# Performance work log

Hardware: AMD Instinct MI355X
Metric: run time of the kernel (lower is better)

## Reference

```python
import jax, jax.numpy as jnp
import numpy as np

B, U, HEADS, S = 16, 1024, 8, 1024


def setup_inputs() -> dict:
    key = jax.random.key(0)
    k1, k2, k3, k4 = jax.random.split(key, 4)
    x = jax.random.normal(k1, (B, U, S), dtype=jnp.float32)
    mask = jax.random.randint(k2, (B, S, S), 0, 2).astype(bool)
    w_qkv = jax.random.normal(k3, (3 * U, U), dtype=jnp.float32) * 0.02
    w_out = jax.random.normal(k4, (U, U), dtype=jnp.float32) * 0.02
    return {"x": x, "mask": mask, "w_qkv": w_qkv, "w_out": w_out}


def reference(x, mask, w_qkv, w_out):
    # x: (B, U, S), mask: (B, n_queries, n_keys) bool
    b, u, s = x.shape
    h = HEADS
    c = u // h  # head (chunk) size
    scale = 1.0 / np.sqrt(c).astype(np.float32)

    # 1x1-conv QKV projection (bias=False): (3U, U) x (B, U, S) -> (B, 3U, S)
    qkv = jnp.einsum('ou,bus->bos', w_qkv, x)
    Q, K, V = jnp.split(qkv, 3, axis=1)           # each (B, U, S)
    Qh = Q.reshape(b, h, c, s)
    Kh = K.reshape(b, h, c, s)
    Vh = V.reshape(b, h, c, s)

    # attention logits: (B, H, n_q, n_k)
    A = jnp.einsum('bhcq,bhck->bhqk', Qh, Kh)

    # relu activation with per-query valid-key-count normalization
    m = mask.sum(axis=2)[:, :, None]              # (B, n_q, 1) count of valid keys
    n_elem = jnp.where(mask, m, 1).astype(A.dtype)[:, None]  # (B, 1, n_q, n_k)
    mask_b = mask[:, None]                        # broadcast over heads
    A = jnp.where(mask_b, jax.nn.relu(A) * scale, -jnp.inf)
    A = A / n_elem
    A = jnp.where(jnp.isinf(A), jnp.zeros((), A.dtype), A)

    # attention-value aggregation (faithful math of broadcast+sum): (B, H, C, n_q)
    Ch = jnp.einsum('bhqk,bhck->bhcq', A, Vh)
    Cc = Ch.reshape(b, u, s)

    # finishing 1x1-conv linear layer
    return jnp.einsum('ou,bus->bos', w_out, Cc)
```

## Files before the change

### kernel.cpp

```cpp
#include <hip/hip_runtime.h>

#define B_DIM 16
#define U_DIM 1024
#define H_DIM 8
#define S_DIM 1024
#define C_DIM 128
#define KD 1024
#define SCALE 0.08838834764831845f

typedef __attribute__((ext_vector_type(8))) short s16x8;
typedef __attribute__((ext_vector_type(4))) float f32x4;

__device__ __forceinline__ void gll16(const void* g, void* l) {
  __builtin_amdgcn_global_load_lds(
      (const __attribute__((address_space(1))) unsigned int*)g,
      (__attribute__((address_space(3))) unsigned int*)l, 16, 0, 0);
}
__device__ __forceinline__ unsigned short f2bf(float f) {
  unsigned u = __float_as_uint(f);
  u += 0x7FFF + ((u >> 16) & 1u);
  return (unsigned short)(u >> 16);
}
#define MFMA16(a, b, c) __builtin_amdgcn_mfma_f32_16x16x32_bf16(a, b, c, 0, 0, 0)

__global__ void detect_mask(const unsigned char* __restrict__ mask_raw, int* __restrict__ flag) {
  __shared__ int not01, notf;
  if (threadIdx.x == 0) { not01 = 0; notf = 0; }
  __syncthreads();
  const unsigned int* p = (const unsigned int*)mask_raw;
  int l01 = 0, lf = 0;
  for (int i = threadIdx.x; i < 4096; i += 256) {
    unsigned int v = p[i];
    if (v != 0u && v != 1u) l01 = 1;
    if (v != 0u && v != 0x3F800000u) lf = 1;
  }
  if (l01) atomicOr(&not01, 1);
  if (lf) atomicOr(&notf, 1);
  __syncthreads();
  if (threadIdx.x == 0) flag[0] = (!not01) ? 0 : ((!notf) ? 2 : 1);
}

__global__ __launch_bounds__(256) void pack_mask(const unsigned char* __restrict__ mask_raw,
                                                 const int* __restrict__ flag,
                                                 unsigned long long* __restrict__ bits) {
  __shared__ unsigned char tile[64][80];
  const int t = threadIdx.x;
  const int kt = blockIdx.x * 64, qw = blockIdx.y, b = blockIdx.z;
  const int mk = flag[0];
  const int q = t >> 2, kbase = (t & 3) * 16;
  const size_t row = (size_t)(b * S_DIM + qw * 64 + q);
  if (mk == 1) {
    uint4 v = *(const uint4*)(mask_raw + (row << 10) + kt + kbase);
    *(uint4*)&tile[q][kbase] = v;
  } else if (mk == 0) {
    const int* p = (const int*)mask_raw + (row << 10) + kt + kbase;
#pragma unroll
    for (int j = 0; j < 4; ++j) {
      int4 v = ((const int4*)p)[j];
      uchar4 o;
      o.x = v.x ? 1 : 0; o.y = v.y ? 1 : 0; o.z = v.z ? 1 : 0; o.w = v.w ? 1 : 0;
      *(uchar4*)&tile[q][kbase + j * 4] = o;
    }
  } else {
    const float* p = (const float*)mask_raw + (row << 10) + kt + kbase;
#pragma unroll
    for (int j = 0; j < 4; ++j) {
      float4 v = ((const float4*)p)[j];
      uchar4 o;
      o.x = (v.x != 0.f) ? 1 : 0; o.y = (v.y != 0.f) ? 1 : 0;
      o.z = (v.z != 0.f) ? 1 : 0; o.w = (v.w != 0.f) ? 1 : 0;
      *(uchar4*)&tile[q][kbase + j * 4] = o;
    }
  }
  __syncthreads();
  const int wave = t >> 6, lane = t & 63;
#pragma unroll
  for (int qq = 0; qq < 16; ++qq) {
    int qr = wave * 16 + qq;
    unsigned long long bal = __ballot(tile[qr][lane] != 0);
    if (lane == 0)
      bits[(size_t)blockIdx.x * (B_DIM * S_DIM) + (size_t)b * S_DIM + qw * 64 + qr] = bal;
  }
}

__global__ __launch_bounds__(256) void invm_from_bits(const unsigned long long* __restrict__ bits,
                                                      float* __restrict__ invm) {
  int idx = blockIdx.x * 256 + threadIdx.x;
  int s = 0;
#pragma unroll
  for (int kt = 0; kt < S_DIM / 64; ++kt)
    s += __popcll(bits[(size_t)kt * (B_DIM * S_DIM) + idx]);
  invm[idx] = (s > 0) ? (SCALE / (float)s) : 0.f;
}

__global__ __launch_bounds__(256) void cvt_bf16(const float* __restrict__ in,
                                                unsigned short* __restrict__ out, int n) {
  int i = (blockIdx.x * 256 + threadIdx.x) * 4;
  if (i < n) {
    float4 v = *(const float4*)(in + i);
    ushort4 o;
    o.x = f2bf(v.x); o.y = f2bf(v.y); o.z = f2bf(v.z); o.w = f2bf(v.w);
    *(ushort4*)(out + i) = o;
  }
}

__global__ __launch_bounds__(256) void transpose_x(const float* __restrict__ x,
                                                   unsigned short* __restrict__ xT) {
  __shared__ float T[32][33];
  const int t = threadIdx.x, r = t >> 3, c4 = (t & 7) * 4;
  const int s0 = blockIdx.x * 32, u0 = blockIdx.y * 32;
  const size_t base = (size_t)blockIdx.z * U_DIM * S_DIM;
  float4 v = *(const float4*)(x + base + (size_t)(u0 + r) * S_DIM + s0 + c4);
  T[r][c4 + 0] = v.x; T[r][c4 + 1] = v.y; T[r][c4 + 2] = v.z; T[r][c4 + 3] = v.w;
  __syncthreads();
  ushort4 o;
  o.x = f2bf(T[c4 + 0][r]); o.y = f2bf(T[c4 + 1][r]);
  o.z = f2bf(T[c4 + 2][r]); o.w = f2bf(T[c4 + 3][r]);
  *(ushort4*)(xT + base + (size_t)(s0 + r) * U_DIM + u0 + c4) = o;
}

__global__ __launch_bounds__(256) void transpose_v(const unsigned short* __restrict__ qkvT,
                                                   unsigned short* __restrict__ VT) {
  __shared__ unsigned short T[32][34];
  const int t = threadIdx.x, r = t >> 3, c4 = (t & 7) * 4;
  const int k0 = blockIdx.x * 32, c0 = blockIdx.y * 32;
  const unsigned short* qb = qkvT + (size_t)blockIdx.z * S_DIM * (3 * U_DIM);
  ushort4 v = *(const ushort4*)(qb + (size_t)(k0 + r) * (3 * U_DIM) + 2 * U_DIM + c0 + c4);
  T[r][c4 + 0] = v.x; T[r][c4 + 1] = v.y; T[r][c4 + 2] = v.z; T[r][c4 + 3] = v.w;
  __syncthreads();
  ushort4 o;
  o.x = T[c4 + 0][r]; o.y = T[c4 + 1][r]; o.z = T[c4 + 2][r]; o.w = T[c4 + 3][r];
  *(ushort4*)(VT + (size_t)blockIdx.z * U_DIM * S_DIM + (size_t)(c0 + r) * S_DIM + k0 + c4) = o;
}

template <typename OUT>
__global__ __launch_bounds__(256) void gemm_tt(const unsigned short* __restrict__ A,
                                               const unsigned short* __restrict__ Bm,
                                               OUT* __restrict__ D,
                                               long long sAb, long long sBb, long long sDb,
                                               int N) {
  __shared__ unsigned short sA[128 * 64];
  __shared__ unsigned short sB[128 * 64];
  const int tid = threadIdx.x, wave = tid >> 6, lane = tid & 63;
  const int l15 = lane & 15, quad = lane >> 4;
  const unsigned int Lb = blockIdx.x + gridDim.x * (blockIdx.y + gridDim.y * blockIdx.z);
  const unsigned int nwg = gridDim.x * gridDim.y * gridDim.z;
  const unsigned int logical = (Lb & 7u) * (nwg >> 3) + (Lb >> 3);
  const int bx = logical % gridDim.x;
  const unsigned int rem = logical / gridDim.x;
  const int by = rem % gridDim.y;
  const int bz = rem / gridDim.y;
  const int m0 = by * 128, n0 = bx * 128;
  A += (size_t)bz * sAb;
  Bm += (size_t)bz * sBb;
  D += (size_t)bz * sDb;
  const int wm = (wave >> 1) * 64, wn = (wave & 1) * 64;
  f32x4 acc[4][4] = {};

  for (int k0 = 0; k0 < KD; k0 += 64) {
#pragma unroll
    for (int t = 0; t < 4; ++t) {
      int p = wave * 256 + t * 64 + lane;
      int row = p >> 3, kc = (p & 7) ^ (row & 7);
      gll16(A + (size_t)(m0 + row) * KD + k0 + kc * 8, &sA[(wave * 256 + t * 64) * 8]);
    }
#pragma unroll
    for (int t = 0; t < 4; ++t) {
      int p = wave * 256 + t * 64 + lane;
      int row = p >> 3, kc = (p & 7) ^ (row & 7);
      gll16(Bm + (size_t)(n0 + row) * KD + k0 + kc * 8, &sB[(wave * 256 + t * 64) * 8]);
    }
    __syncthreads();
#pragma unroll
    for (int kk = 0; kk < 2; ++kk) {
      s16x8 af[4], bf[4];
#pragma unroll
      for (int i = 0; i < 4; ++i) {
        int row = wm + i * 16 + l15;
        af[i] = *(const s16x8*)&sA[row * 64 + ((kk * 4 + quad) ^ (row & 7)) * 8];
      }
#pragma unroll
      for (int j = 0; j < 4; ++j) {
        int row = wn + j * 16 + l15;
        bf[j] = *(const s16x8*)&sB[row * 64 + ((kk * 4 + quad) ^ (row & 7)) * 8];
      }
#pragma unroll
      for (int i = 0; i < 4; ++i)
#pragma unroll
        for (int j = 0; j < 4; ++j) acc[i][j] = MFMA16(af[i], bf[j], acc[i][j]);
    }
    __syncthreads();
  }
#pragma unroll
  for (int i = 0; i < 4; ++i)
#pragma unroll
    for (int j = 0; j < 4; ++j) {
      f32x4 v = acc[i][j];
#pragma unroll
      for (int r = 0; r < 4; ++r) {
        int m = m0 + wm + i * 16 + quad * 4 + r;
        int n = n0 + wn + j * 16 + l15;
        if constexpr (sizeof(OUT) == 2) D[(size_t)m * N + n] = f2bf(v[r]);
        else D[(size_t)m * N + n] = v[r];
      }
    }
}

__global__ __launch_bounds__(256, 2) void attn_mfma(const unsigned short* __restrict__ qkvT,
                                                    const unsigned short* __restrict__ VT,
                                                    const unsigned long long* __restrict__ bits,
                                                    const float* __restrict__ invm,
                                                    unsigned short* __restrict__ CcT, int b0) {
  __shared__ unsigned short QV[64 * 128];
  __shared__ unsigned short Ks[64 * 128];
  __shared__ unsigned short Vs[128 * 64];
  __shared__ unsigned short Ps[64 * 64];
  __shared__ float invs[64];

  const int tid = threadIdx.x, wave = tid >> 6, lane = tid & 63;
  const int l15 = lane & 15, quad = lane >> 4;
  const int L = blockIdx.x + 16 * (blockIdx.y + 8 * blockIdx.z);
  const int cpx = (16 * H_DIM * gridDim.z) >> 3;
  const int logical = (L & 7) * cpx + (L >> 3);
  const int qt = logical & 15, h = (logical >> 4) & 7, z = logical >> 7;
  const int q0 = qt * 64, b = b0 + z;
  const unsigned short* qB = qkvT + (size_t)z * S_DIM * (3 * U_DIM);
  const unsigned short* Vb = VT + (size_t)z * U_DIM * S_DIM + (size_t)h * C_DIM * S_DIM;

#pragma unroll
  for (int t = 0; t < 4; ++t) {
    int p = wave * 256 + t * 64 + lane;
    int row = p >> 4, c = (p & 15) ^ (row & 7);
    gll16(qB + (size_t)(q0 + row) * (3 * U_DIM) + h * C_DIM + c * 8,
          &QV[(wave * 256 + t * 64) * 8]);
    gll16(qB + (size_t)(row) * (3 * U_DIM) + U_DIM + h * C_DIM + c * 8,
          &Ks[(wave * 256 + t * 64) * 8]);
    int vrow = p >> 3, vkc = (p & 7) ^ (vrow & 7);
    gll16(Vb + (size_t)vrow * S_DIM + vkc * 8, &Vs[(wave * 256 + t * 64) * 8]);
  }
  if (tid < 64) invs[tid] = invm[(size_t)b * S_DIM + q0 + tid];
  __syncthreads();

  s16x8 qf[4][4];
#pragma unroll
  for (int j = 0; j < 4; ++j)
#pragma unroll
    for (int kk = 0; kk < 4; ++kk) {
      int row = j * 16 + l15;
      qf[j][kk] = *(const s16x8*)&QV[row * 128 + ((kk * 4 + quad) ^ (row & 7)) * 8];
    }
  float invf[4];
#pragma unroll
  for (int j = 0; j < 4; ++j) invf[j] = invs[j * 16 + l15];

  f32x4 pacc[4][2] = {};

  for (int kt = 0; kt < S_DIM / 64; ++kt) {
    unsigned long long w64[4];
    {
      const unsigned long long* mw =
          bits + (size_t)kt * (B_DIM * S_DIM) + (size_t)b * S_DIM + q0;
#pragma unroll
      for (int j = 0; j < 4; ++j) w64[j] = mw[j * 16 + l15];
    }

    s16x8 af[4];
#pragma unroll
    for (int kk = 0; kk < 4; ++kk) {
      int row = wave * 16 + l15;
      af[kk] = *(const s16x8*)&Ks[row * 128 + ((kk * 4 + quad) ^ (row & 7)) * 8];
    }
    f32x4 sacc[4] = {};
    __builtin_amdgcn_s_setprio(1);
#pragma unroll
    for (int kk = 0; kk < 4; ++kk)
#pragma unroll
      for (int j = 0; j < 4; ++j) sacc[j] = MFMA16(af[kk], qf[j][kk], sacc[j]);
    __builtin_amdgcn_s_setprio(0);

#pragma unroll
    for (int j = 0; j < 4; ++j) {
      const unsigned int m4 = (unsigned int)(w64[j] >> (wave * 16 + quad * 4)) & 0xFu;
      float p[4];
#pragma unroll
      for (int r = 0; r < 4; ++r) {
        float t = fmaxf(sacc[j][r], 0.f) * invf[j];
        p[r] = ((m4 >> r) & 1u) ? t : 0.f;
      }
      unsigned int pk0, pk1;
      asm("v_cvt_pk_bf16_f32 %0, %1, %2" : "=v"(pk0) : "v"(p[0]), "v"(p[1]));
      asm("v_cvt_pk_bf16_f32 %0, %1, %2" : "=v"(pk1) : "v"(p[2]), "v"(p[3]));
      int q = j * 16 + l15;
      int chunk = (wave * 2 + (quad >> 1)) ^ (q & 7);
      *(uint2*)&Ps[q * 64 + chunk * 8 + (quad & 1) * 4] = make_uint2(pk0, pk1);
    }
    __syncthreads();

    if (kt < S_DIM / 64 - 1) {
      const int kn = (kt + 1) * 64;
      unsigned short* vdst = (kt & 1) ? Vs : QV;
#pragma unroll
      for (int t = 0; t < 4; ++t) {
        int p = wave * 256 + t * 64 + lane;
        int row = p >> 4, c = (p & 15) ^ (row & 7);
        gll16(qB + (size_t)(kn + row) * (3 * U_DIM) + U_DIM + h * C_DIM + c * 8,
              &Ks[(wave * 256 + t * 64) * 8]);
        int vrow = p >> 3, vkc = (p & 7) ^ (vrow & 7);
        gll16(Vb + (size_t)vrow * S_DIM + kn + vkc * 8, &vdst[(wave * 256 + t * 64) * 8]);
      }
    }

    const unsigned short* vbuf = (kt & 1) ? QV : Vs;
#pragma unroll
    for (int ks = 0; ks < 2; ++ks) {
      s16x8 pf[4], vf[2];
#pragma unroll
      for (int i = 0; i < 4; ++i) {
        int row = i * 16 + l15;
        pf[i] = *(const s16x8*)&Ps[row * 64 + ((ks * 4 + quad) ^ (row & 7)) * 8];
      }
#pragma unroll
      for (int j = 0; j < 2; ++j) {
        int row = wave * 32 + j * 16 + l15;
        vf[j] = *(const s16x8*)&vbuf[row * 64 + ((ks * 4 + quad) ^ (row & 7)) * 8];
      }
      __builtin_amdgcn_s_setprio(1);
#pragma unroll
      for (int i = 0; i < 4; ++i)
#pragma unroll
        for (int j = 0; j < 2; ++j) pacc[i][j] = MFMA16(pf[i], vf[j], pacc[i][j]);
      __builtin_amdgcn_s_setprio(0);
    }
    __syncthreads();
  }

  unsigned short* cb = CcT + (size_t)z * S_DIM * U_DIM;
#pragma unroll
  for (int i = 0; i < 4; ++i)
#pragma unroll
    for (int j = 0; j < 2; ++j) {
      f32x4 v = pacc[i][j];
#pragma unroll
      for (int r = 0; r < 4; ++r) {
        int q = q0 + i * 16 + quad * 4 + r;
        int c = h * C_DIM + wave * 32 + j * 16 + l15;
        cb[(size_t)q * U_DIM + c] = f2bf(v[r]);
      }
    }
}

extern "C" void kernel_launch(void* const* d_in, const int* in_sizes, int n_in,
                              void* d_out, int out_size, void* d_ws, size_t ws_size,
                              hipStream_t stream) {
  const float* x = (const float*)d_in[0];
  const unsigned char* mask_raw = (const unsigned char*)d_in[1];
  const float* w_qkv = (const float*)d_in[2];
  const float* w_out = (const float*)d_in[3];
  float* out = (float*)d_out;

  char* ws = (char*)d_ws;
  int* flag = (int*)ws;
  float* invm = (float*)(ws + 256);
  unsigned long long* bits = (unsigned long long*)(ws + 256 + 65536);
  unsigned short* wqkv_bf = (unsigned short*)((char*)bits + (size_t)B_DIM * S_DIM * 16 * 8);
  unsigned short* wout_bf = (unsigned short*)((char*)wqkv_bf + (size_t)3 * U_DIM * U_DIM * 2);
  char* heap = (char*)wout_bf + (size_t)U_DIM * U_DIM * 2;

  const size_t xT_pb = (size_t)U_DIM * S_DIM * 2;
  const size_t qkvT_pb = (size_t)3 * U_DIM * S_DIM * 2;
  const size_t vT_pb = (size_t)U_DIM * S_DIM * 2;
  const size_t ccT_pb = (size_t)U_DIM * S_DIM * 2;
  const size_t per_batch = xT_pb + qkvT_pb + vT_pb + ccT_pb;
  const size_t fixed = (size_t)(heap - ws);
  int nb = (ws_size > fixed) ? (int)((ws_size - fixed) / per_batch) : 1;
  if (nb < 1) nb = 1;
  if (nb > B_DIM) nb = B_DIM;

  unsigned short* xT = (unsigned short*)heap;
  unsigned short* qkvT = (unsigned short*)(heap + (size_t)nb * xT_pb);
  unsigned short* VT = (unsigned short*)(heap + (size_t)nb * (xT_pb + qkvT_pb));
  unsigned short* CcT = (unsigned short*)(heap + (size_t)nb * (xT_pb + qkvT_pb + vT_pb));

  detect_mask<<<1, 256, 0, stream>>>(mask_raw, flag);
  pack_mask<<<dim3(S_DIM / 64, S_DIM / 64, B_DIM), 256, 0, stream>>>(mask_raw, flag, bits);
  invm_from_bits<<<(B_DIM * S_DIM) / 256, 256, 0, stream>>>(bits, invm);
  cvt_bf16<<<(3 * U_DIM * U_DIM) / 1024, 256, 0, stream>>>(w_qkv, wqkv_bf, 3 * U_DIM * U_DIM);
  cvt_bf16<<<(U_DIM * U_DIM) / 1024, 256, 0, stream>>>(w_out, wout_bf, U_DIM * U_DIM);

  for (int b0 = 0; b0 < B_DIM; b0 += nb) {
    int cnt = (B_DIM - b0 < nb) ? (B_DIM - b0) : nb;
    transpose_x<<<dim3(S_DIM / 32, U_DIM / 32, cnt), 256, 0, stream>>>(
        x + (size_t)b0 * U_DIM * S_DIM, xT);
    gemm_tt<unsigned short><<<dim3(3 * U_DIM / 128, S_DIM / 128, cnt), 256, 0, stream>>>(
        xT, wqkv_bf, qkvT, (long long)U_DIM * S_DIM, 0LL, (long long)3 * U_DIM * S_DIM, 3 * U_DIM);
    transpose_v<<<dim3(S_DIM / 32, U_DIM / 32, cnt), 256, 0, stream>>>(qkvT, VT);
    attn_mfma<<<dim3(S_DIM / 64, H_DIM, cnt), 256, 0, stream>>>(
        qkvT, VT, bits, invm, CcT, b0);
    gemm_tt<float><<<dim3(S_DIM / 128, U_DIM / 128, cnt), 256, 0, stream>>>(
        wout_bf, CcT, out + (size_t)b0 * U_DIM * S_DIM, 0LL,
        (long long)U_DIM * S_DIM, (long long)U_DIM * S_DIM, S_DIM);
  }
}
```

Before: 484.7 us.

## Replace GEMMs with 256x256-tile, 512-thread, triple-buffered LDS pipeline

Both projection GEMMs move from a 128x128-tile, 256-thread kernel that loads and syncs every K step to a 256x256-tile, 512-thread kernel. The new kernel uses K=32 stages held in three LDS buffers, prefetched two steps ahead with partial vmcnt waits. It also raises wave priority around the MFMA block. The goal is to hide global-to-LDS latency behind compute and get more operand reuse per tile, at the cost of 96KB LDS, more accumulator registers, and fewer workgroups per launch.

```diff
diff --git a/kernel.cpp b/kernel.cpp
--- a/kernel.cpp
+++ b/kernel.cpp
@@ -133,16 +133,49 @@
   *(ushort4*)(VT + (size_t)blockIdx.z * U_DIM * S_DIM + (size_t)(c0 + r) * S_DIM + k0 + c4) = o;
 }
 
+__device__ __forceinline__ void g256_stage(const unsigned short* pA0, const unsigned short* pA1,
+                                           const unsigned short* pB0, const unsigned short* pB1,
+                                           int k0, int tid,
+                                           unsigned short* dA, unsigned short* dB) {
+  gll16(pA0 + k0, dA + (size_t)tid * 8);
+  gll16(pB0 + k0, dB + (size_t)tid * 8);
+  gll16(pA1 + k0, dA + (size_t)(512 + tid) * 8);
+  gll16(pB1 + k0, dB + (size_t)(512 + tid) * 8);
+}
+
+__device__ __forceinline__ void g256_tile(const unsigned short* sa, const unsigned short* sb,
+                                          int wm, int wn, int l15, int quad, f32x4 acc[8][4]) {
+  s16x8 af[8], bf[4];
+#pragma unroll
+  for (int i = 0; i < 8; ++i) {
+    int r = wm * 128 + i * 16 + l15;
+    af[i] = *(const s16x8*)&sa[r * 32 + ((quad ^ ((r >> 1) & 3)) * 8)];
+  }
+#pragma unroll
+  for (int j = 0; j < 4; ++j) {
+    int r = wn * 64 + j * 16 + l15;
+    bf[j] = *(const s16x8*)&sb[r * 32 + ((quad ^ ((r >> 1) & 3)) * 8)];
+  }
+  __builtin_amdgcn_s_setprio(1);
+#pragma unroll
+  for (int i = 0; i < 8; ++i)
+#pragma unroll
+    for (int j = 0; j < 4; ++j) acc[i][j] = MFMA16(af[i], bf[j], acc[i][j]);
+  __builtin_amdgcn_s_setprio(0);
+}
+
 template <typename OUT>
-__global__ __launch_bounds__(256) void gemm_tt(const unsigned short* __restrict__ A,
-                                               const unsigned short* __restrict__ Bm,
-                                               OUT* __restrict__ D,
-                                               long long sAb, long long sBb, long long sDb,
-                                               int N) {
-  __shared__ unsigned short sA[128 * 64];
-  __shared__ unsigned short sB[128 * 64];
-  const int tid = threadIdx.x, wave = tid >> 6, lane = tid & 63;
+__global__ __launch_bounds__(512, 2) void gemm256(const unsigned short* __restrict__ A,
+                                                  const unsigned short* __restrict__ Bm,
+                                                  OUT* __restrict__ D,
+                                                  long long sAb, long long sBb, long long sDb,
+                                                  int N) {
+  __shared__ unsigned short sA0[256 * 32], sA1[256 * 32], sA2[256 * 32];
+  __shared__ unsigned short sB0[256 * 32], sB1[256 * 32], sB2[256 * 32];
+  const int tid = threadIdx.x;
+  const int wave = tid >> 6, lane = tid & 63;
   const int l15 = lane & 15, quad = lane >> 4;
+  const int wm = wave >> 2, wn = wave & 3;
   const unsigned int Lb = blockIdx.x + gridDim.x * (blockIdx.y + gridDim.y * blockIdx.z);
   const unsigned int nwg = gridDim.x * gridDim.y * gridDim.z;
   const unsigned int logical = (Lb & 7u) * (nwg >> 3) + (Lb >> 3);
@@ -150,56 +183,55 @@
   const unsigned int rem = logical / gridDim.x;
   const int by = rem % gridDim.y;
   const int bz = rem / gridDim.y;
-  const int m0 = by * 128, n0 = bx * 128;
-  A += (size_t)bz * sAb;
-  Bm += (size_t)bz * sBb;
+  const int m0 = by * 256, n0 = bx * 256;
+  A += (size_t)bz * sAb + (size_t)m0 * KD;
+  Bm += (size_t)bz * sBb + (size_t)n0 * KD;
   D += (size_t)bz * sDb;
-  const int wm = (wave >> 1) * 64, wn = (wave & 1) * 64;
-  f32x4 acc[4][4] = {};
-
-  for (int k0 = 0; k0 < KD; k0 += 64) {
-#pragma unroll
-    for (int t = 0; t < 4; ++t) {
-      int p = wave * 256 + t * 64 + lane;
-      int row = p >> 3, kc = (p & 7) ^ (row & 7);
-      gll16(A + (size_t)(m0 + row) * KD + k0 + kc * 8, &sA[(wave * 256 + t * 64) * 8]);
-    }
-#pragma unroll
-    for (int t = 0; t < 4; ++t) {
-      int p = wave * 256 + t * 64 + lane;
-      int row = p >> 3, kc = (p & 7) ^ (row & 7);
-      gll16(Bm + (size_t)(n0 + row) * KD + k0 + kc * 8, &sB[(wave * 256 + t * 64) * 8]);
-    }
-    __syncthreads();
-#pragma unroll
-    for (int kk = 0; kk < 2; ++kk) {
-      s16x8 af[4], bf[4];
-#pragma unroll
-      for (int i = 0; i < 4; ++i) {
-        int row = wm + i * 16 + l15;
-        af[i] = *(const s16x8*)&sA[row * 64 + ((kk * 4 + quad) ^ (row & 7)) * 8];
-      }
-#pragma unroll
-      for (int j = 0; j < 4; ++j) {
-        int row = wn + j * 16 + l15;
-        bf[j] = *(const s16x8*)&sB[row * 64 + ((kk * 4 + quad) ^ (row & 7)) * 8];
-      }
-#pragma unroll
-      for (int i = 0; i < 4; ++i)
-#pragma unroll
-        for (int j = 0; j < 4; ++j) acc[i][j] = MFMA16(af[i], bf[j], acc[i][j]);
-    }
-    __syncthreads();
-  }
-#pragma unroll
-  for (int i = 0; i < 4; ++i)
+
+  const int g0 = tid, g1 = 512 + tid;
+  const int rA0 = g0 >> 2, rA1 = g1 >> 2;
+  const int kc0 = (g0 & 3) ^ ((rA0 >> 1) & 3), kc1 = (g1 & 3) ^ ((rA1 >> 1) & 3);
+  const unsigned short* pA0 = A + (size_t)rA0 * KD + kc0 * 8;
+  const unsigned short* pA1 = A + (size_t)rA1 * KD + kc1 * 8;
+  const unsigned short* pB0 = Bm + (size_t)rA0 * KD + kc0 * 8;
+  const unsigned short* pB1 = Bm + (size_t)rA1 * KD + kc1 * 8;
+
+  f32x4 acc[8][4] = {};
+
+  g256_stage(pA0, pA1, pB0, pB1, 0, tid, sA0, sB0);
+  g256_stage(pA0, pA1, pB0, pB1, 32, tid, sA1, sB1);
+  asm volatile("s_waitcnt vmcnt(4)" ::: "memory");
+  __builtin_amdgcn_s_barrier();
+
+#define G256_STEP(T, SAc, SBc, SAn, SBn, DO_STAGE, WAITN)                      \
+  {                                                                            \
+    if (DO_STAGE) g256_stage(pA0, pA1, pB0, pB1, ((T) + 2) * 32, tid, SAn, SBn); \
+    g256_tile(SAc, SBc, wm, wn, l15, quad, acc);                               \
+    if ((WAITN) >= 0) {                                                        \
+      if ((WAITN) == 4) asm volatile("s_waitcnt vmcnt(4)" ::: "memory");       \
+      else asm volatile("s_waitcnt vmcnt(0)" ::: "memory");                    \
+      __builtin_amdgcn_s_barrier();                                            \
+    }                                                                          \
+  }
+
+  for (int tt = 0; tt < 30; tt += 3) {
+    G256_STEP(tt + 0, sA0, sB0, sA2, sB2, 1, 4);
+    G256_STEP(tt + 1, sA1, sB1, sA0, sB0, 1, 4);
+    G256_STEP(tt + 2, sA2, sB2, sA1, sB1, 1, 4);
+  }
+  G256_STEP(30, sA0, sB0, sA2, sB2, 0, 0);
+  G256_STEP(31, sA1, sB1, sA2, sB2, 0, -1);
+#undef G256_STEP
+
+#pragma unroll
+  for (int i = 0; i < 8; ++i)
 #pragma unroll
     for (int j = 0; j < 4; ++j) {
       f32x4 v = acc[i][j];
 #pragma unroll
       for (int r = 0; r < 4; ++r) {
-        int m = m0 + wm + i * 16 + quad * 4 + r;
-        int n = n0 + wn + j * 16 + l15;
+        int m = m0 + wm * 128 + i * 16 + quad * 4 + r;
+        int n = n0 + wn * 64 + j * 16 + l15;
         if constexpr (sizeof(OUT) == 2) D[(size_t)m * N + n] = f2bf(v[r]);
         else D[(size_t)m * N + n] = v[r];
       }
@@ -391,12 +423,12 @@
     int cnt = (B_DIM - b0 < nb) ? (B_DIM - b0) : nb;
     transpose_x<<<dim3(S_DIM / 32, U_DIM / 32, cnt), 256, 0, stream>>>(
         x + (size_t)b0 * U_DIM * S_DIM, xT);
-    gemm_tt<unsigned short><<<dim3(3 * U_DIM / 128, S_DIM / 128, cnt), 256, 0, stream>>>(
+    gemm256<unsigned short><<<dim3(3 * U_DIM / 256, S_DIM / 256, cnt), 512, 0, stream>>>(
         xT, wqkv_bf, qkvT, (long long)U_DIM * S_DIM, 0LL, (long long)3 * U_DIM * S_DIM, 3 * U_DIM);
     transpose_v<<<dim3(S_DIM / 32, U_DIM / 32, cnt), 256, 0, stream>>>(qkvT, VT);
     attn_mfma<<<dim3(S_DIM / 64, H_DIM, cnt), 256, 0, stream>>>(
         qkvT, VT, bits, invm, CcT, b0);
-    gemm_tt<float><<<dim3(S_DIM / 128, U_DIM / 128, cnt), 256, 0, stream>>>(
+    gemm256<float><<<dim3(S_DIM / 256, U_DIM / 256, cnt), 512, 0, stream>>>(
         wout_bf, CcT, out + (size_t)b0 * U_DIM * S_DIM, 0LL,
         (long long)U_DIM * S_DIM, (long long)U_DIM * S_DIM, S_DIM);
   }
```

Measured after the change: 465.0 us. 1.04x faster.

## Replace GEMM with 256x256 double-buffered pipelined MFMA kernel

Applied to the files above, without the earlier changes.

Replaces the 128x128 single-buffered GEMM used for the QKV and output projections with a 256x256 tile, 512-thread kernel. It double-buffers the A and B tiles in LDS and interleaves global-to-LDS loads for the next K tile between MFMA phases, using explicit vmcnt waits and barriers plus s_setprio around the MFMA bursts. The aim is to hide load latency and raise arithmetic intensity per block. The cost is 128KB of LDS per block and larger accumulator register use, which limits occupancy. The grid is smaller, so wave quantization across CUs could be worse.

```diff
diff --git a/kernel.cpp b/kernel.cpp
--- a/kernel.cpp
+++ b/kernel.cpp
@@ -134,15 +134,17 @@
 }
 
 template <typename OUT>
-__global__ __launch_bounds__(256) void gemm_tt(const unsigned short* __restrict__ A,
-                                               const unsigned short* __restrict__ Bm,
-                                               OUT* __restrict__ D,
-                                               long long sAb, long long sBb, long long sDb,
-                                               int N) {
-  __shared__ unsigned short sA[128 * 64];
-  __shared__ unsigned short sB[128 * 64];
-  const int tid = threadIdx.x, wave = tid >> 6, lane = tid & 63;
+__global__ __launch_bounds__(512, 2) void gemm256(const unsigned short* __restrict__ A,
+                                                  const unsigned short* __restrict__ Bm,
+                                                  OUT* __restrict__ D,
+                                                  long long sAb, long long sBb, long long sDb,
+                                                  int N) {
+  __shared__ unsigned short sA0[256 * 64], sB0[256 * 64];
+  __shared__ unsigned short sA1[256 * 64], sB1[256 * 64];
+  const int tid = threadIdx.x;
+  const int wave = tid >> 6, lane = tid & 63;
   const int l15 = lane & 15, quad = lane >> 4;
+  const int wm = wave & 3, wn = wave >> 2;
   const unsigned int Lb = blockIdx.x + gridDim.x * (blockIdx.y + gridDim.y * blockIdx.z);
   const unsigned int nwg = gridDim.x * gridDim.y * gridDim.z;
   const unsigned int logical = (Lb & 7u) * (nwg >> 3) + (Lb >> 3);
@@ -150,56 +152,123 @@
   const unsigned int rem = logical / gridDim.x;
   const int by = rem % gridDim.y;
   const int bz = rem / gridDim.y;
-  const int m0 = by * 128, n0 = bx * 128;
-  A += (size_t)bz * sAb;
-  Bm += (size_t)bz * sBb;
+  const int m0 = by * 256, n0 = bx * 256;
+  A += (size_t)bz * sAb + (size_t)m0 * KD;
+  Bm += (size_t)bz * sBb + (size_t)n0 * KD;
   D += (size_t)bz * sDb;
-  const int wm = (wave >> 1) * 64, wn = (wave & 1) * 64;
-  f32x4 acc[4][4] = {};
-
-  for (int k0 = 0; k0 < KD; k0 += 64) {
-#pragma unroll
-    for (int t = 0; t < 4; ++t) {
-      int p = wave * 256 + t * 64 + lane;
-      int row = p >> 3, kc = (p & 7) ^ (row & 7);
-      gll16(A + (size_t)(m0 + row) * KD + k0 + kc * 8, &sA[(wave * 256 + t * 64) * 8]);
-    }
-#pragma unroll
-    for (int t = 0; t < 4; ++t) {
-      int p = wave * 256 + t * 64 + lane;
-      int row = p >> 3, kc = (p & 7) ^ (row & 7);
-      gll16(Bm + (size_t)(n0 + row) * KD + k0 + kc * 8, &sB[(wave * 256 + t * 64) * 8]);
-    }
-    __syncthreads();
-#pragma unroll
-    for (int kk = 0; kk < 2; ++kk) {
-      s16x8 af[4], bf[4];
-#pragma unroll
-      for (int i = 0; i < 4; ++i) {
-        int row = wm + i * 16 + l15;
-        af[i] = *(const s16x8*)&sA[row * 64 + ((kk * 4 + quad) ^ (row & 7)) * 8];
-      }
-#pragma unroll
-      for (int j = 0; j < 4; ++j) {
-        int row = wn + j * 16 + l15;
-        bf[j] = *(const s16x8*)&sB[row * 64 + ((kk * 4 + quad) ^ (row & 7)) * 8];
-      }
-#pragma unroll
-      for (int i = 0; i < 4; ++i)
-#pragma unroll
-        for (int j = 0; j < 4; ++j) acc[i][j] = MFMA16(af[i], bf[j], acc[i][j]);
-    }
-    __syncthreads();
-  }
+
+  const int r0 = tid >> 3;
+  const int kc0 = (tid & 7) ^ (r0 & 7);
+  const unsigned short* pA = A + (size_t)r0 * KD + kc0 * 8;
+  const unsigned short* pB = Bm + (size_t)r0 * KD + kc0 * 8;
+  const int wo = wave * 512;
+
+#define STG_U0(SA, K0)                                        \
+  do {                                                        \
+    gll16(pA + (K0), &(SA)[wo]);                              \
+    gll16(pA + 64 * KD + (K0), &(SA)[4096 + wo]);             \
+  } while (0)
+#define STG_U1(SA, K0)                                        \
+  do {                                                        \
+    gll16(pA + 128 * KD + (K0), &(SA)[8192 + wo]);            \
+    gll16(pA + 192 * KD + (K0), &(SA)[12288 + wo]);           \
+  } while (0)
+#define STG_U2(SB, K0)                                        \
+  do {                                                        \
+    gll16(pB + (K0), &(SB)[wo]);                              \
+    gll16(pB + 128 * KD + (K0), &(SB)[8192 + wo]);            \
+  } while (0)
+#define STG_U3(SB, K0)                                        \
+  do {                                                        \
+    gll16(pB + 64 * KD + (K0), &(SB)[4096 + wo]);             \
+    gll16(pB + 192 * KD + (K0), &(SB)[12288 + wo]);           \
+  } while (0)
+
+#define WAITB(VN)                                             \
+  do {                                                        \
+    asm volatile("s_waitcnt vmcnt(" #VN ")" ::: "memory");    \
+    __builtin_amdgcn_s_barrier();                             \
+    asm volatile("" ::: "memory");                            \
+  } while (0)
+
+  s16x8 a[4][2];
+  f32x4 acc[4][8] = {};
+
+#define LDA(SA)                                                                         \
+  do {                                                                                  \
+    _Pragma("unroll") for (int i = 0; i < 4; ++i) {                                     \
+      int row = wm * 64 + i * 16 + l15;                                                 \
+      _Pragma("unroll") for (int ks = 0; ks < 2; ++ks)                                  \
+          a[i][ks] = *(const s16x8*)&(SA)[row * 64 + (((ks * 4 + quad) ^ (row & 7)) * 8)]; \
+    }                                                                                   \
+  } while (0)
+
+#define PHASE(SB, P)                                                                    \
+  do {                                                                                  \
+    s16x8 b[2][2];                                                                      \
+    _Pragma("unroll") for (int jj = 0; jj < 2; ++jj) {                                  \
+      int row = wn * 128 + ((P) * 2 + jj) * 16 + l15;                                   \
+      _Pragma("unroll") for (int ks = 0; ks < 2; ++ks)                                  \
+          b[jj][ks] = *(const s16x8*)&(SB)[row * 64 + (((ks * 4 + quad) ^ (row & 7)) * 8)]; \
+    }                                                                                   \
+    __builtin_amdgcn_s_setprio(1);                                                      \
+    _Pragma("unroll") for (int ks = 0; ks < 2; ++ks)                                    \
+        _Pragma("unroll") for (int i = 0; i < 4; ++i)                                   \
+            _Pragma("unroll") for (int jj = 0; jj < 2; ++jj)                            \
+                acc[i][(P) * 2 + jj] = MFMA16(a[i][ks], b[jj][ks], acc[i][(P) * 2 + jj]); \
+    __builtin_amdgcn_s_setprio(0);                                                      \
+  } while (0)
+
+#define TILE(SA, SB, SAn, SBn, K1)                            \
+  do {                                                        \
+    WAITB(2);                                                 \
+    STG_U0(SAn, K1);                                          \
+    LDA(SA);                                                  \
+    PHASE(SB, 0);                                             \
+    STG_U1(SAn, K1);                                          \
+    PHASE(SB, 1);                                             \
+    WAITB(4);                                                 \
+    STG_U2(SBn, K1);                                          \
+    PHASE(SB, 2);                                             \
+    STG_U3(SBn, K1);                                          \
+    PHASE(SB, 3);                                             \
+  } while (0)
+
+  STG_U0(sA0, 0); STG_U1(sA0, 0); STG_U2(sB0, 0); STG_U3(sB0, 0);
+
+  for (int kt = 0; kt < 14; kt += 2) {
+    TILE(sA0, sB0, sA1, sB1, (kt + 1) * 64);
+    TILE(sA1, sB1, sA0, sB0, (kt + 2) * 64);
+  }
+  TILE(sA0, sB0, sA1, sB1, 15 * 64);
+
+  {
+    WAITB(2);
+    LDA(sA1);
+    PHASE(sB1, 0);
+    PHASE(sB1, 1);
+    WAITB(0);
+    PHASE(sB1, 2);
+    PHASE(sB1, 3);
+  }
+#undef TILE
+#undef PHASE
+#undef LDA
+#undef WAITB
+#undef STG_U0
+#undef STG_U1
+#undef STG_U2
+#undef STG_U3
+
 #pragma unroll
   for (int i = 0; i < 4; ++i)
 #pragma unroll
-    for (int j = 0; j < 4; ++j) {
+    for (int j = 0; j < 8; ++j) {
       f32x4 v = acc[i][j];
 #pragma unroll
       for (int r = 0; r < 4; ++r) {
-        int m = m0 + wm + i * 16 + quad * 4 + r;
-        int n = n0 + wn + j * 16 + l15;
+        int m = m0 + wm * 64 + i * 16 + quad * 4 + r;
+        int n = n0 + wn * 128 + j * 16 + l15;
         if constexpr (sizeof(OUT) == 2) D[(size_t)m * N + n] = f2bf(v[r]);
         else D[(size_t)m * N + n] = v[r];
       }
@@ -391,12 +460,12 @@
     int cnt = (B_DIM - b0 < nb) ? (B_DIM - b0) : nb;
     transpose_x<<<dim3(S_DIM / 32, U_DIM / 32, cnt), 256, 0, stream>>>(
         x + (size_t)b0 * U_DIM * S_DIM, xT);
-    gemm_tt<unsigned short><<<dim3(3 * U_DIM / 128, S_DIM / 128, cnt), 256, 0, stream>>>(
+    gemm256<unsigned short><<<dim3(3 * U_DIM / 256, S_DIM / 256, cnt), 512, 0, stream>>>(
         xT, wqkv_bf, qkvT, (long long)U_DIM * S_DIM, 0LL, (long long)3 * U_DIM * S_DIM, 3 * U_DIM);
     transpose_v<<<dim3(S_DIM / 32, U_DIM / 32, cnt), 256, 0, stream>>>(qkvT, VT);
     attn_mfma<<<dim3(S_DIM / 64, H_DIM, cnt), 256, 0, stream>>>(
         qkvT, VT, bits, invm, CcT, b0);
-    gemm_tt<float><<<dim3(S_DIM / 128, U_DIM / 128, cnt), 256, 0, stream>>>(
+    gemm256<float><<<dim3(S_DIM / 256, U_DIM / 256, cnt), 512, 0, stream>>>(
         wout_bf, CcT, out + (size_t)b0 * U_DIM * S_DIM, 0LL,
         (long long)U_DIM * S_DIM, (long long)U_DIM * S_DIM, S_DIM);
   }
```

Measured after the change: 462.0 us. 4.7% less time.
